# Performance work log

Hardware: AMD Instinct MI355X
Metric: run time of the kernel (lower is better)

## Reference

```python
import jax, jax.numpy as jnp
import numpy as np

B, Ng, A, Eg = 32, 2500, 50, 2000      # graphs, atoms/graph, residues/graph, edges/graph
DIN, EDIM, H1, H2, AF, HG = 64, 16, 64, 64, 95, 128
F1, F2, F3 = 64, 32, 16
K, T = 3, 6                             # ARMA num_stacks, num_layers
N, E = B * Ng, B * Eg


def _glorot(k, shape, fan_in):
    return jax.random.normal(k, shape, jnp.float32) / np.sqrt(fan_in)


def setup_inputs():
    key = jax.random.key(0)
    ks = jax.random.split(key, 24)
    x = jax.random.normal(ks[0], (N, DIN), jnp.float32)
    off = (jnp.arange(B) * Ng)[:, None]
    src = (jax.random.randint(ks[1], (B, Eg), 0, Ng) + off).reshape(-1)
    dst = (jax.random.randint(ks[2], (B, Eg), 0, Ng) + off).reshape(-1)
    edge_index = jnp.stack([src, dst])
    edge_attr = jax.random.normal(ks[3], (E, EDIM), jnp.float32)
    monomer_labels = jnp.tile(jnp.arange(Ng) // (Ng // A), B)  # atom -> residue (0..A-1, per graph)
    aminoacids_features = jax.random.normal(ks[4], (B, A, AF), jnp.float32)
    FIN = H2 + AF  # 159, ARMA input dim
    return {
        'x': x, 'edge_index': edge_index, 'edge_attr': edge_attr,
        'monomer_labels': monomer_labels, 'aminoacids_features': aminoacids_features,
        'w_e1': _glorot(ks[5], (EDIM, DIN * H1), EDIM), 'b_e1': jnp.zeros((DIN * H1,)),
        'root1': _glorot(ks[6], (DIN, H1), DIN), 'bias1': jnp.zeros((H1,)),
        'w_e2': _glorot(ks[7], (EDIM, H1 * H2), EDIM), 'b_e2': jnp.zeros((H1 * H2,)),
        'root2': _glorot(ks[8], (H1, H2), H1), 'bias2': jnp.zeros((H2,)),
        'attn_atom_w': _glorot(ks[9], (H2, 1), H2), 'attn_atom_b': jnp.zeros((1,)),
        'arma_init_w': _glorot(ks[10], (K, FIN, HG), FIN),
        'arma_w': _glorot(ks[11], (T - 1, K, HG, HG), HG),
        'arma_root_w': _glorot(ks[12], (T, K, FIN, HG), FIN),
        'arma_bias': jnp.zeros((T, K, 1, HG)),
        'attn_aa_w': _glorot(ks[13], (HG, 1), HG), 'attn_aa_b': jnp.zeros((1,)),
        'w1': _glorot(ks[14], (HG, F1), HG), 'b1': jnp.zeros((F1,)),
        'w2': _glorot(ks[15], (F1, F2), F1), 'b2': jnp.zeros((F2,)),
        'w3': _glorot(ks[16], (F2, F3), F2), 'b3': jnp.zeros((F3,)),
        'w4': _glorot(ks[17], (F3, 1), F3), 'b4': jnp.zeros((1,)),
    }


def reference(x, edge_index, edge_attr, monomer_labels, aminoacids_features,
              w_e1, b_e1, root1, bias1, w_e2, b_e2, root2, bias2,
              attn_atom_w, attn_atom_b, arma_init_w, arma_w, arma_root_w, arma_bias,
              attn_aa_w, attn_aa_b, w1, b1, w2, b2, w3, b3, w4, b4):
    src, dst = edge_index[0], edge_index[1]

    def nnconv(h, w_e, b_e, root, bias):
        din, dout = root.shape
        W = (edge_attr @ w_e + b_e).reshape(-1, din, dout)      # per-edge weight [E, din, dout]
        msg = jnp.einsum('ei,eio->eo', h[src], W)               # per-edge matvec
        agg = jax.ops.segment_sum(msg, dst, num_segments=N)     # scatter-add at dst
        return agg + h @ root + bias

    h = jax.nn.relu(nnconv(x, w_e1, b_e1, root1, bias1))
    h = jax.nn.relu(nnconv(h, w_e2, b_e2, root2, bias2))

    # AttentionReadoutAtom per graph: softmax over atoms, scatter-sum to residues
    hb = h.reshape(B, Ng, H2)
    attn = jax.nn.softmax(hb @ attn_atom_w + attn_atom_b, axis=1)
    wx = (hb * attn).reshape(-1, H2)
    seg = (monomer_labels.reshape(B, Ng) + jnp.arange(B)[:, None] * A).reshape(-1)
    amino = jax.ops.segment_sum(wx, seg, num_segments=B * A).reshape(B, A, H2)
    xi = jnp.concatenate([amino, aminoacids_features], axis=-1)  # [B, A, H2+95]

    # ARMAConv over directed residue chain i->i+1; gcn_norm w/o self-loops:
    # node 0 has in-degree 0 so edge (0,1) gets norm 0, all others norm 1.
    norm = jnp.concatenate([jnp.zeros(1), jnp.ones(A - 2)])      # [A-1]

    def prop(z):  # z: [B, K, A, F]; out[i+1] = norm_i * z[i]
        shifted = z[..., :-1, :] * norm[:, None]
        return jnp.concatenate([jnp.zeros_like(z[..., :1, :]), shifted], axis=-2)

    out = prop(jnp.einsum('baf,kfg->bkag', xi, arma_init_w))
    out = jax.nn.relu(out + jnp.einsum('baf,kfg->bkag', xi, arma_root_w[0]) + arma_bias[0][None])
    for t in range(1, T):
        out = prop(jnp.einsum('bkaf,kfg->bkag', out, arma_w[t - 1]))
        out = jax.nn.relu(out + jnp.einsum('baf,kfg->bkag', xi, arma_root_w[t]) + arma_bias[t][None])
    g = jax.nn.relu(out.mean(axis=1))  # mean over K stacks -> [B, A, HG]

    # AttentionReadoutAminoAcid: softmax over residues, weighted sum
    a = jax.nn.softmax(g @ attn_aa_w + attn_aa_b, axis=1)
    p = (g * a).sum(axis=1)  # [B, HG]

    # MLP head (dropout is identity in eval mode)
    p = jax.nn.relu(p @ w1 + b1)
    p = jax.nn.relu(p @ w2 + b2)
    p = jax.nn.relu(p @ w3 + b3)
    return (p @ w4 + b4).reshape(-1)
```

## Files before the change

kernel.cpp:

```cpp
#include <hip/hip_runtime.h>

#define N_NODES 80000
#define N_EDGES 64000
#define NB      32
#define NG      2500
#define NA      50
#define EDIM    16
#define FIN     159
#define HG      128
#define RICOLS  2688
#define XSTR    132

typedef __attribute__((ext_vector_type(8))) short bf16x8;
typedef __attribute__((ext_vector_type(4))) float f32x4;

__device__ inline ushort rne_bf16(float f) {
    union { float f; unsigned u; } v; v.f = f;
    const unsigned r = v.u + 0x7fffu + ((v.u >> 16) & 1u);
    return (ushort)(r >> 16);
}
__device__ inline float bf16_to_f32(ushort h) {
    union { unsigned u; float f; } v; v.u = ((unsigned)h) << 16;
    return v.f;
}
__device__ __forceinline__ void gl_lds16(const void* gsrc, void* ldst) {
    __builtin_amdgcn_global_load_lds(
        (const __attribute__((address_space(1))) unsigned int*)gsrc,
        (__attribute__((address_space(3))) unsigned int*)ldst, 16, 0, 0);
}

__global__ __launch_bounds__(256) void prep_w2(const float* __restrict__ we1, const float* __restrict__ be1,
    const float* __restrict__ we2, const float* __restrict__ be2,
    ushort* __restrict__ w1h, ushort* __restrict__ w1l, ushort* __restrict__ w2h, ushort* __restrict__ w2l)
{
    int idx = blockIdx.x * 256 + threadIdx.x;
    const int half = (idx >= 17 * 8 * 64) ? 1 : 0;
    if (half) idx -= 17 * 8 * 64;
    if (idx >= 17 * 8 * 64) return;
    const float* we = half ? we2 : we1;
    const float* be = half ? be2 : be1;
    ushort* Wh = half ? w2h : w1h;
    ushort* Wlo = half ? w2l : w1l;
    const int l = idx & 63;
    const int slot = (idx >> 6) & 7;
    const int j = idx >> 9;
    const int n = slot >> 1, kq = slot & 1;
    const int o = n * 16 + (l & 15);
    const int i0 = kq * 32 + (l >> 4) * 8;
    ushort th[8], tl[8];
#pragma unroll
    for (int t = 0; t < 8; ++t) {
        const int i = i0 + t;
        const float f = (j < 16) ? we[j * 4096 + i * 64 + o] : be[i * 64 + o];
        const ushort hi = rne_bf16(f);
        th[t] = hi;
        tl[t] = rne_bf16(f - bf16_to_f32(hi));
    }
    *(uint4*)(Wh + (size_t)idx * 8) = *(const uint4*)th;
    *(uint4*)(Wlo + (size_t)idx * 8) = *(const uint4*)tl;
}

__global__ __launch_bounds__(256) void prep_arma(const float* __restrict__ armaw,
    ushort* __restrict__ Bh, ushort* __restrict__ Bl)
{
    const int idx = blockIdx.x * 256 + threadIdx.x;
    if (idx >= 15 * 32 * 64) return;
    const int l = idx & 63;
    const int slot = (idx >> 6) & 31;
    const int ws = idx >> 11;
    const int n = slot >> 2, kt = slot & 3;
    const int c = n * 16 + (l & 15);
    const int f0 = kt * 32 + (l >> 4) * 8;
    ushort th[8], tl[8];
#pragma unroll
    for (int t = 0; t < 8; ++t) {
        const float v = armaw[(size_t)ws * 16384 + (size_t)(f0 + t) * 128 + c];
        const ushort hi = rne_bf16(v);
        th[t] = hi;
        tl[t] = rne_bf16(v - bf16_to_f32(hi));
    }
    *(uint4*)(Bh + (size_t)idx * 8) = *(const uint4*)th;
    *(uint4*)(Bl + (size_t)idx * 8) = *(const uint4*)tl;
}

template<int RELU>
__global__ __launch_bounds__(256) void root_gemm(const float* __restrict__ in,
    const float* __restrict__ w, const float* __restrict__ bias, float* __restrict__ out)
{
    __shared__ float At[64 * 65];
    __shared__ float Wl[64 * 64];
    __shared__ float bl[64];
    const int tid = threadIdx.x;
    const int r0 = blockIdx.x * 64;
    for (int s = tid; s < 4096; s += 256) {
        int r = s >> 6, c = s & 63;
        float v = in[(r0 + r) * 64 + c];
        if (RELU) v = fmaxf(v, 0.f);
        At[c * 65 + r] = v;
    }
    for (int s = tid; s < 4096; s += 256) Wl[s] = w[s];
    if (tid < 64) bl[tid] = bias[tid];
    __syncthreads();
    const int tr = tid >> 4, tc = tid & 15;
    float acc[4][4] = {};
#pragma unroll 8
    for (int i = 0; i < 64; ++i) {
        const float4 a4 = *(const float4*)&At[i * 65 + tr * 4];
        const float4 b4 = *(const float4*)&Wl[i * 64 + tc * 4];
        const float av[4] = {a4.x, a4.y, a4.z, a4.w};
        const float bv[4] = {b4.x, b4.y, b4.z, b4.w};
#pragma unroll
        for (int m = 0; m < 4; ++m)
#pragma unroll
            for (int n = 0; n < 4; ++n) acc[m][n] = fmaf(av[m], bv[n], acc[m][n]);
    }
    const float4 bq = *(const float4*)&bl[tc * 4];
#pragma unroll
    for (int m = 0; m < 4; ++m) {
        float4 o4 = {acc[m][0] + bq.x, acc[m][1] + bq.y, acc[m][2] + bq.z, acc[m][3] + bq.w};
        *(float4*)&out[(r0 + tr * 4 + m) * 64 + tc * 4] = o4;
    }
}

#define TE 128
template<int RELU>
__global__ __launch_bounds__(256) void edge_conv_mfma(const float* __restrict__ h,
    const float* __restrict__ ea, const int* __restrict__ src, const int* __restrict__ dst,
    const ushort* __restrict__ Whi, const ushort* __restrict__ Wlo, float* __restrict__ agg)
{
    __shared__ ushort Bst[2][8192];
    __shared__ float  EAt[17 * 132];
    const int tid = threadIdx.x;
    const int e0 = blockIdx.x * TE;
    const int wv = tid >> 6, l = tid & 63;

#pragma unroll
    for (int i = 0; i < 4; ++i) {
        const int c = wv * 4 + i;
        const ushort* gs = (c < 8) ? (Whi + ((size_t)c * 64 + l) * 8)
                                   : (Wlo + ((size_t)(c - 8) * 64 + l) * 8);
        gl_lds16(gs, (char*)(&Bst[0][0]) + c * 1024);
    }
    for (int s = tid; s < TE * 16; s += 256) {
        const int le = s >> 4, j = s & 15;
        EAt[j * 132 + le] = ea[(size_t)(e0 + le) * 16 + j];
    }
    if (tid < TE) EAt[16 * 132 + tid] = 1.0f;

    bf16x8 ah[2][2], al[2][2];
#pragma unroll
    for (int m = 0; m < 2; ++m) {
        const int erow = wv * 32 + m * 16 + (l & 15);
        const int nd = src[e0 + erow];
        const float4* hp = (const float4*)(h + (size_t)nd * 64);
#pragma unroll
        for (int kq = 0; kq < 2; ++kq) {
            const int q0 = kq * 8 + (l >> 4) * 2;
            const float4 v0 = hp[q0], v1 = hp[q0 + 1];
            const float fv[8] = {v0.x, v0.y, v0.z, v0.w, v1.x, v1.y, v1.z, v1.w};
            ushort th[8], tl[8];
#pragma unroll
            for (int t = 0; t < 8; ++t) {
                const float f = RELU ? fmaxf(fv[t], 0.f) : fv[t];
                th[t] = rne_bf16(f);
                tl[t] = rne_bf16(f - bf16_to_f32(th[t]));
            }
            ah[m][kq] = *(const bf16x8*)th;
            al[m][kq] = *(const bf16x8*)tl;
        }
    }
    __syncthreads();

    f32x4 msg[2][4];
#pragma unroll
    for (int m = 0; m < 2; ++m)
#pragma unroll
        for (int n = 0; n < 4; ++n) msg[m][n] = (f32x4)0.f;

#pragma unroll 1
    for (int j = 0; j < 17; ++j) {
        const int cur = j & 1;
        if (j < 16) {
#pragma unroll
            for (int i = 0; i < 4; ++i) {
                const int c = wv * 4 + i;
                const ushort* gs = (c < 8) ? (Whi + ((size_t)((j + 1) * 8 + c) * 64 + l) * 8)
                                           : (Wlo + ((size_t)((j + 1) * 8 + (c - 8)) * 64 + l) * 8);
                gl_lds16(gs, (char*)(&Bst[cur ^ 1][0]) + c * 1024);
            }
        }
        f32x4 eam[2];
        eam[0] = *(const f32x4*)&EAt[j * 132 + wv * 32 + (l >> 4) * 4];
        eam[1] = *(const f32x4*)&EAt[j * 132 + wv * 32 + 16 + (l >> 4) * 4];
#pragma unroll
        for (int n = 0; n < 4; ++n) {
            const char* bb = (const char*)(&Bst[cur][0]);
            const bf16x8 bh0 = *(const bf16x8*)(bb + ((n * 2 + 0) * 64 + l) * 16);
            const bf16x8 bh1 = *(const bf16x8*)(bb + ((n * 2 + 1) * 64 + l) * 16);
            const bf16x8 bl0 = *(const bf16x8*)(bb + 8192 + ((n * 2 + 0) * 64 + l) * 16);
            const bf16x8 bl1 = *(const bf16x8*)(bb + 8192 + ((n * 2 + 1) * 64 + l) * 16);
#pragma unroll
            for (int m = 0; m < 2; ++m) {
                f32x4 t = __builtin_amdgcn_mfma_f32_16x16x32_bf16(ah[m][0], bh0, (f32x4)0.f, 0, 0, 0);
                t = __builtin_amdgcn_mfma_f32_16x16x32_bf16(ah[m][1], bh1, t, 0, 0, 0);
                t = __builtin_amdgcn_mfma_f32_16x16x32_bf16(ah[m][0], bl0, t, 0, 0, 0);
                t = __builtin_amdgcn_mfma_f32_16x16x32_bf16(ah[m][1], bl1, t, 0, 0, 0);
                t = __builtin_amdgcn_mfma_f32_16x16x32_bf16(al[m][0], bh0, t, 0, 0, 0);
                t = __builtin_amdgcn_mfma_f32_16x16x32_bf16(al[m][1], bh1, t, 0, 0, 0);
                msg[m][n] += eam[m] * t;
            }
        }
        __syncthreads();
    }

#pragma unroll
    for (int m = 0; m < 2; ++m)
#pragma unroll
        for (int r = 0; r < 4; ++r) {
            const int erow = wv * 32 + m * 16 + (l >> 4) * 4 + r;
            const size_t d = (size_t)dst[e0 + erow] * 64;
#pragma unroll
            for (int n = 0; n < 4; ++n)
                atomicAdd(&agg[d + n * 16 + (l & 15)], msg[m][n][r]);
        }
}

__global__ __launch_bounds__(256) void scores_k(const float* __restrict__ h2,
    const float* __restrict__ w, const float* __restrict__ b, float* __restrict__ sc)
{
    __shared__ float wl[64];
    if (threadIdx.x < 64) wl[threadIdx.x] = w[threadIdx.x];
    __syncthreads();
    const int n = blockIdx.x * 256 + threadIdx.x;
    if (n < N_NODES) {
        float acc = b[0];
        const float4* hp = (const float4*)(h2 + (long)n * 64);
#pragma unroll
        for (int q = 0; q < 16; ++q) {
            const float4 v = hp[q];
            acc = fmaf(fmaxf(v.x, 0.f), wl[q * 4 + 0], acc); acc = fmaf(fmaxf(v.y, 0.f), wl[q * 4 + 1], acc);
            acc = fmaf(fmaxf(v.z, 0.f), wl[q * 4 + 2], acc); acc = fmaf(fmaxf(v.w, 0.f), wl[q * 4 + 3], acc);
        }
        sc[n] = acc;
    }
}

__global__ __launch_bounds__(256) void softmax_k(const float* __restrict__ sc, float* __restrict__ attn)
{
    __shared__ float red[256];
    const int g = blockIdx.x, tid = threadIdx.x;
    const float* s = sc + (long)g * NG;
    float m = -1e30f;
    for (int a = tid; a < NG; a += 256) m = fmaxf(m, s[a]);
    red[tid] = m; __syncthreads();
    for (int st = 128; st; st >>= 1) { if (tid < st) red[tid] = fmaxf(red[tid], red[tid + st]); __syncthreads(); }
    const float mx = red[0]; __syncthreads();
    float sum = 0.f;
    for (int a = tid; a < NG; a += 256) sum += expf(s[a] - mx);
    red[tid] = sum; __syncthreads();
    for (int st = 128; st; st >>= 1) { if (tid < st) red[tid] += red[tid + st]; __syncthreads(); }
    const float inv = 1.0f / red[0];
    for (int a = tid; a < NG; a += 256) attn[(long)g * NG + a] = expf(s[a] - mx) * inv;
}

__global__ __launch_bounds__(256) void amino_k(const float* __restrict__ h2,
    const float* __restrict__ attn, const float* __restrict__ aa, float* __restrict__ xi)
{
    const int tid = threadIdx.x;
    const int r = blockIdx.x * 4 + (tid >> 6);
    const int o = tid & 63;
    const int g = r / NA, ar = r % NA;
    const long base = (long)g * NG + ar * 50;
    float acc = 0.f;
#pragma unroll 10
    for (int a = 0; a < 50; ++a) acc = fmaf(attn[base + a], fmaxf(h2[(base + a) * 64 + o], 0.f), acc);
    xi[(long)r * FIN + o] = acc;
    for (int s = tid; s < 4 * 95; s += 256) {
        const int lr = s / 95, f = s % 95;
        const int rr = blockIdx.x * 4 + lr;
        xi[(long)rr * FIN + 64 + f] = aa[(long)rr * 95 + f];
    }
}

__global__ __launch_bounds__(256) void ri_gemm(const float* __restrict__ xi,
    const float* __restrict__ rootw, const float* __restrict__ initw,
    const float* __restrict__ abias, float* __restrict__ RI)
{
    __shared__ float At[32 * 65];
    __shared__ float Bl[32 * 64];
    const int tid = threadIdx.x;
    const int r0 = blockIdx.x * 64, c0 = blockIdx.y * 64;
    const int blk = c0 >> 7;
    const int gb = c0 & 127;
    const float* bsrc = (blk < 18) ? (rootw + (long)blk * FIN * 128) : (initw + (long)(blk - 18) * FIN * 128);
    const int tr = tid >> 4, tc = tid & 15;
    float acc[4][4] = {};
    for (int f0 = 0; f0 < FIN; f0 += 32) {
        __syncthreads();
        for (int s = tid; s < 64 * 32; s += 256) {
            const int r = s >> 5, kk = s & 31; const int f = f0 + kk;
            At[kk * 65 + r] = (f < FIN) ? xi[(long)(r0 + r) * FIN + f] : 0.f;
        }
        for (int s = tid; s < 32 * 64; s += 256) {
            const int kk = s >> 6, cc = s & 63; const int f = f0 + kk;
            Bl[s] = (f < FIN) ? bsrc[(long)f * 128 + gb + cc] : 0.f;
        }
        __syncthreads();
#pragma unroll 8
        for (int kk = 0; kk < 32; ++kk) {
            const float4 a4 = *(const float4*)&At[kk * 65 + tr * 4];
            const float4 b4 = *(const float4*)&Bl[kk * 64 + tc * 4];
            const float av[4] = {a4.x, a4.y, a4.z, a4.w};
            const float bv[4] = {b4.x, b4.y, b4.z, b4.w};
#pragma unroll
            for (int m = 0; m < 4; ++m)
#pragma unroll
                for (int n = 0; n < 4; ++n) acc[m][n] = fmaf(av[m], bv[n], acc[m][n]);
        }
    }
    float4 bq = {0.f, 0.f, 0.f, 0.f};
    if (blk < 18) bq = *(const float4*)&abias[c0 + tc * 4];
#pragma unroll
    for (int m = 0; m < 4; ++m) {
        float4 o4 = {acc[m][0] + bq.x, acc[m][1] + bq.y, acc[m][2] + bq.z, acc[m][3] + bq.w};
        *(float4*)&RI[(long)(r0 + tr * 4 + m) * RICOLS + c0 + tc * 4] = o4;
    }
}

__global__ __launch_bounds__(128) void arma_all(const float* __restrict__ RI,
    const ushort* __restrict__ Bh, const ushort* __restrict__ Bl, float* __restrict__ G)
{
    __shared__ float Xl[2][32 * XSTR];
    const int bid = blockIdx.x;
    const int g = bid / 6, k = (bid % 6) >> 1, half = bid & 1;
    const int tid = threadIdx.x;
    const int r0 = half ? 20 : 0;
    const size_t rbase = (size_t)g * NA;

    for (int s = tid; s < 30 * 128; s += 128) {
        const int lr = s >> 7, o = s & 127;
        const int a = r0 + lr;
        float v = RI[(rbase + a) * RICOLS + k * 128 + o];
        if (a >= 2) v += RI[(rbase + a - 1) * RICOLS + (18 + k) * 128 + o];
        Xl[0][lr * XSTR + o] = fmaxf(v, 0.f);
    }
    for (int s = tid; s < 2 * 128; s += 128) {
        const int lr = 30 + (s >> 7), o = s & 127;
        Xl[0][lr * XSTR + o] = 0.f;
        Xl[1][lr * XSTR + o] = 0.f;
    }

    const int wv = tid >> 6, l = tid & 63;
    const int arow = wv * 16 + (l & 15);
    const bool avalid = (arow >= 1) && (r0 + arow >= 2);
    const int asrc = avalid ? (arow - 1) : 0;
    int cur = 0;

    for (int t = 1; t <= 5; ++t) {
        __syncthreads();
        bf16x8 ah[4], al[4];
#pragma unroll
        for (int kt = 0; kt < 4; ++kt) {
            const float* xp = &Xl[cur][asrc * XSTR + kt * 32 + (l >> 4) * 8];
            const float4 v0 = *(const float4*)xp;
            const float4 v1 = *(const float4*)(xp + 4);
            const float fv[8] = {v0.x, v0.y, v0.z, v0.w, v1.x, v1.y, v1.z, v1.w};
            ushort th[8], tl[8];
#pragma unroll
            for (int t8 = 0; t8 < 8; ++t8) {
                const float f = avalid ? fv[t8] : 0.f;
                th[t8] = rne_bf16(f);
                tl[t8] = rne_bf16(f - bf16_to_f32(th[t8]));
            }
            ah[kt] = *(const bf16x8*)th;
            al[kt] = *(const bf16x8*)tl;
        }
        const size_t wsbase = (size_t)(((t - 1) * 3 + k) * 32) * 64 * 8;
#pragma unroll
        for (int n = 0; n < 8; ++n) {
            f32x4 acc = (f32x4)0.f;
#pragma unroll
            for (int kt = 0; kt < 4; ++kt) {
                const size_t fo = wsbase + (size_t)(n * 4 + kt) * 64 * 8 + (size_t)l * 8;
                const bf16x8 bh = *(const bf16x8*)(Bh + fo);
                const bf16x8 bl8 = *(const bf16x8*)(Bl + fo);
                acc = __builtin_amdgcn_mfma_f32_16x16x32_bf16(ah[kt], bh, acc, 0, 0, 0);
                acc = __builtin_amdgcn_mfma_f32_16x16x32_bf16(ah[kt], bl8, acc, 0, 0, 0);
                acc = __builtin_amdgcn_mfma_f32_16x16x32_bf16(al[kt], bh, acc, 0, 0, 0);
            }
            const int cn = n * 16 + (l & 15);
#pragma unroll
            for (int r = 0; r < 4; ++r) {
                const int lr = wv * 16 + (l >> 4) * 4 + r;
                if (lr < 30) {
                    const float rv = RI[(rbase + r0 + lr) * RICOLS + (t * 3 + k) * 128 + cn];
                    Xl[cur ^ 1][lr * XSTR + cn] = fmaxf(acc[r] + rv, 0.f);
                }
            }
        }
        cur ^= 1;
    }
    __syncthreads();
    const int w0 = half ? 25 : 0;
    for (int s = tid; s < 25 * 128; s += 128) {
        const int a = w0 + (s >> 7), o = s & 127;
        G[((size_t)k * 1600 + rbase + a) * 128 + o] = Xl[cur][(a - r0) * XSTR + o];
    }
}

__global__ __launch_bounds__(256) void final_k(const float* __restrict__ G,
    const float* __restrict__ waa, const float* __restrict__ baa,
    const float* __restrict__ w1, const float* __restrict__ b1,
    const float* __restrict__ w2, const float* __restrict__ b2,
    const float* __restrict__ w3, const float* __restrict__ b3,
    const float* __restrict__ w4, const float* __restrict__ b4, float* __restrict__ out)
{
    __shared__ float gl[50 * 129];
    __shared__ float sc[64];
    __shared__ float pl[128];
    __shared__ float h1l[64], h2l[32], h3l[16];
    __shared__ float wl[128];
    const int b = blockIdx.x, tid = threadIdx.x;
    for (int s = tid; s < 50 * 128; s += 256) {
        const int a = s >> 7, o = s & 127;
        const size_t r = ((size_t)b * 50 + a) * 128 + o;
        const float v = (G[r] + G[(size_t)1600 * 128 + r] + G[(size_t)2 * 1600 * 128 + r]) * (1.f / 3.f);
        gl[a * 129 + o] = fmaxf(v, 0.f);
    }
    if (tid < 128) wl[tid] = waa[tid];
    __syncthreads();
    if (tid < 50) {
        float acc = baa[0];
        for (int f = 0; f < 128; ++f) acc = fmaf(gl[tid * 129 + f], wl[f], acc);
        sc[tid] = acc;
    }
    __syncthreads();
    if (tid < 64) {
        const float v = (tid < 50) ? sc[tid] : -1e30f;
        float m = v;
        for (int d = 32; d; d >>= 1) m = fmaxf(m, __shfl_xor(m, d));
        const float e = (tid < 50) ? expf(v - m) : 0.f;
        float ssum = e;
        for (int d = 32; d; d >>= 1) ssum += __shfl_xor(ssum, d);
        if (tid < 50) sc[tid] = e / ssum;
    }
    __syncthreads();
    if (tid < 128) {
        float acc = 0.f;
        for (int a = 0; a < 50; ++a) acc = fmaf(sc[a], gl[a * 129 + tid], acc);
        pl[tid] = acc;
    }
    __syncthreads();
    if (tid < 64) {
        float acc = b1[tid];
        for (int f = 0; f < 128; ++f) acc = fmaf(pl[f], w1[f * 64 + tid], acc);
        h1l[tid] = fmaxf(acc, 0.f);
    }
    __syncthreads();
    if (tid < 32) {
        float acc = b2[tid];
        for (int f = 0; f < 64; ++f) acc = fmaf(h1l[f], w2[f * 32 + tid], acc);
        h2l[tid] = fmaxf(acc, 0.f);
    }
    __syncthreads();
    if (tid < 16) {
        float acc = b3[tid];
        for (int f = 0; f < 32; ++f) acc = fmaf(h2l[f], w3[f * 16 + tid], acc);
        h3l[tid] = fmaxf(acc, 0.f);
    }
    __syncthreads();
    if (tid == 0) {
        float acc = b4[0];
        for (int f = 0; f < 16; ++f) acc = fmaf(h3l[f], w4[f], acc);
        out[b] = acc;
    }
}

extern "C" void kernel_launch(void* const* d_in, const int* in_sizes, int n_in,
                              void* d_out, int out_size, void* d_ws, size_t ws_size,
                              hipStream_t stream) {
    const float* x     = (const float*)d_in[0];
    const int*   eidx  = (const int*)d_in[1];
    const float* ea    = (const float*)d_in[2];
    const float* aaf   = (const float*)d_in[4];
    const float* we1   = (const float*)d_in[5];
    const float* be1   = (const float*)d_in[6];
    const float* root1 = (const float*)d_in[7];
    const float* bias1 = (const float*)d_in[8];
    const float* we2   = (const float*)d_in[9];
    const float* be2   = (const float*)d_in[10];
    const float* root2 = (const float*)d_in[11];
    const float* bias2 = (const float*)d_in[12];
    const float* waw   = (const float*)d_in[13];
    const float* wab   = (const float*)d_in[14];
    const float* initw = (const float*)d_in[15];
    const float* armaw = (const float*)d_in[16];
    const float* rootw = (const float*)d_in[17];
    const float* abias = (const float*)d_in[18];
    const float* waa   = (const float*)d_in[19];
    const float* baa   = (const float*)d_in[20];
    const float* w1    = (const float*)d_in[21];
    const float* b1    = (const float*)d_in[22];
    const float* w2    = (const float*)d_in[23];
    const float* b2    = (const float*)d_in[24];
    const float* w3    = (const float*)d_in[25];
    const float* b3    = (const float*)d_in[26];
    const float* w4    = (const float*)d_in[27];
    const float* b4    = (const float*)d_in[28];
    float* out = (float*)d_out;

    const int* src = eidx;
    const int* dst = eidx + N_EDGES;

    char* ws = (char*)d_ws;
    size_t off = 0;
    float* h1     = (float*)(ws + off); off += (size_t)N_NODES * 64 * 4;
    float* h2     = (float*)(ws + off); off += (size_t)N_NODES * 64 * 4;
    float* scores = (float*)(ws + off); off += (size_t)N_NODES * 4;
    float* attn   = (float*)(ws + off); off += (size_t)N_NODES * 4;
    float* xi     = (float*)(ws + off); off += (size_t)1600 * FIN * 4;
    float* RI     = (float*)(ws + off); off += (size_t)1600 * RICOLS * 4;
    float* G      = (float*)(ws + off); off += (size_t)3 * 1600 * 128 * 4;
    ushort* wt1h  = (ushort*)(ws + off); off += (size_t)17 * 8 * 64 * 8 * 2;
    ushort* wt1l  = (ushort*)(ws + off); off += (size_t)17 * 8 * 64 * 8 * 2;
    ushort* wt2h  = (ushort*)(ws + off); off += (size_t)17 * 8 * 64 * 8 * 2;
    ushort* wt2l  = (ushort*)(ws + off); off += (size_t)17 * 8 * 64 * 8 * 2;
    ushort* abh   = (ushort*)(ws + off); off += (size_t)15 * 32 * 64 * 8 * 2;
    ushort* abl   = (ushort*)(ws + off); off += (size_t)15 * 32 * 64 * 8 * 2;

    prep_w2<<<68, 256, 0, stream>>>(we1, be1, we2, be2, wt1h, wt1l, wt2h, wt2l);
    prep_arma<<<120, 256, 0, stream>>>(armaw, abh, abl);

    root_gemm<0><<<N_NODES / 64, 256, 0, stream>>>(x, root1, bias1, h1);
    edge_conv_mfma<0><<<N_EDGES / TE, 256, 0, stream>>>(x, ea, src, dst, wt1h, wt1l, h1);
    root_gemm<1><<<N_NODES / 64, 256, 0, stream>>>(h1, root2, bias2, h2);
    edge_conv_mfma<1><<<N_EDGES / TE, 256, 0, stream>>>(h1, ea, src, dst, wt2h, wt2l, h2);
    scores_k<<<(N_NODES + 255) / 256, 256, 0, stream>>>(h2, waw, wab, scores);
    softmax_k<<<NB, 256, 0, stream>>>(scores, attn);
    amino_k<<<1600 / 4, 256, 0, stream>>>(h2, attn, aaf, xi);
    ri_gemm<<<dim3(25, 42), 256, 0, stream>>>(xi, rootw, initw, abias, RI);
    arma_all<<<NB * 6, 128, 0, stream>>>(RI, abh, abl, G);
    final_k<<<NB, 256, 0, stream>>>(G, waa, baa, w1, b1, w2, b2, w3, b3, w4, b4, out);
}
```

Baseline: 386.8 us.

## Split ARMA recurrence into single-wave halo chunks and merge weight prep kernels

The ARMA stack kernel is restructured from 192 two-wave blocks with double-buffered LDS and block barriers into 480 single-wave blocks. Each block owns 11 residues plus a 5-row halo, recomputing overlapping rows so that no __syncthreads is needed. The MFMA loop is reordered so that all eight column tiles' B fragments are loaded per k-step and eight independent accumulators are kept, which exposes more instruction-level parallelism at the cost of registers and redundant halo work. The two weight-preparation kernels are also fused into one launch to cut launch overhead.

```diff
diff --git a/kernel.cpp b/kernel.cpp
--- a/kernel.cpp
+++ b/kernel.cpp
@@ -9,7 +9,6 @@
 #define FIN     159
 #define HG      128
 #define RICOLS  2688
-#define XSTR    132
 
 typedef __attribute__((ext_vector_type(8))) short bf16x8;
 typedef __attribute__((ext_vector_type(4))) float f32x4;
@@ -29,58 +28,58 @@
         (__attribute__((address_space(3))) unsigned int*)ldst, 16, 0, 0);
 }
 
-__global__ __launch_bounds__(256) void prep_w2(const float* __restrict__ we1, const float* __restrict__ be1,
-    const float* __restrict__ we2, const float* __restrict__ be2,
-    ushort* __restrict__ w1h, ushort* __restrict__ w1l, ushort* __restrict__ w2h, ushort* __restrict__ w2l)
-{
-    int idx = blockIdx.x * 256 + threadIdx.x;
-    const int half = (idx >= 17 * 8 * 64) ? 1 : 0;
-    if (half) idx -= 17 * 8 * 64;
-    if (idx >= 17 * 8 * 64) return;
-    const float* we = half ? we2 : we1;
-    const float* be = half ? be2 : be1;
-    ushort* Wh = half ? w2h : w1h;
-    ushort* Wlo = half ? w2l : w1l;
-    const int l = idx & 63;
-    const int slot = (idx >> 6) & 7;
-    const int j = idx >> 9;
-    const int n = slot >> 1, kq = slot & 1;
-    const int o = n * 16 + (l & 15);
-    const int i0 = kq * 32 + (l >> 4) * 8;
-    ushort th[8], tl[8];
-#pragma unroll
-    for (int t = 0; t < 8; ++t) {
-        const int i = i0 + t;
-        const float f = (j < 16) ? we[j * 4096 + i * 64 + o] : be[i * 64 + o];
-        const ushort hi = rne_bf16(f);
-        th[t] = hi;
-        tl[t] = rne_bf16(f - bf16_to_f32(hi));
-    }
-    *(uint4*)(Wh + (size_t)idx * 8) = *(const uint4*)th;
-    *(uint4*)(Wlo + (size_t)idx * 8) = *(const uint4*)tl;
-}
-
-__global__ __launch_bounds__(256) void prep_arma(const float* __restrict__ armaw,
-    ushort* __restrict__ Bh, ushort* __restrict__ Bl)
-{
-    const int idx = blockIdx.x * 256 + threadIdx.x;
-    if (idx >= 15 * 32 * 64) return;
-    const int l = idx & 63;
-    const int slot = (idx >> 6) & 31;
-    const int ws = idx >> 11;
-    const int n = slot >> 2, kt = slot & 3;
-    const int c = n * 16 + (l & 15);
-    const int f0 = kt * 32 + (l >> 4) * 8;
-    ushort th[8], tl[8];
-#pragma unroll
-    for (int t = 0; t < 8; ++t) {
-        const float v = armaw[(size_t)ws * 16384 + (size_t)(f0 + t) * 128 + c];
-        const ushort hi = rne_bf16(v);
-        th[t] = hi;
-        tl[t] = rne_bf16(v - bf16_to_f32(hi));
-    }
-    *(uint4*)(Bh + (size_t)idx * 8) = *(const uint4*)th;
-    *(uint4*)(Bl + (size_t)idx * 8) = *(const uint4*)tl;
+__global__ __launch_bounds__(256) void prep_all(const float* __restrict__ we1, const float* __restrict__ be1,
+    const float* __restrict__ we2, const float* __restrict__ be2, const float* __restrict__ armaw,
+    ushort* __restrict__ w1h, ushort* __restrict__ w1l, ushort* __restrict__ w2h, ushort* __restrict__ w2l,
+    ushort* __restrict__ abh, ushort* __restrict__ abl)
+{
+    const int b = blockIdx.x;
+    if (b < 68) {
+        int idx = b * 256 + threadIdx.x;
+        const int half = (idx >= 17 * 8 * 64) ? 1 : 0;
+        if (half) idx -= 17 * 8 * 64;
+        if (idx >= 17 * 8 * 64) return;
+        const float* we = half ? we2 : we1;
+        const float* be = half ? be2 : be1;
+        ushort* Wh = half ? w2h : w1h;
+        ushort* Wlo = half ? w2l : w1l;
+        const int l = idx & 63;
+        const int slot = (idx >> 6) & 7;
+        const int j = idx >> 9;
+        const int n = slot >> 1, kq = slot & 1;
+        const int o = n * 16 + (l & 15);
+        const int i0 = kq * 32 + (l >> 4) * 8;
+        ushort th[8], tl[8];
+#pragma unroll
+        for (int t = 0; t < 8; ++t) {
+            const int i = i0 + t;
+            const float f = (j < 16) ? we[j * 4096 + i * 64 + o] : be[i * 64 + o];
+            const ushort hi = rne_bf16(f);
+            th[t] = hi;
+            tl[t] = rne_bf16(f - bf16_to_f32(hi));
+        }
+        *(uint4*)(Wh + (size_t)idx * 8) = *(const uint4*)th;
+        *(uint4*)(Wlo + (size_t)idx * 8) = *(const uint4*)tl;
+    } else {
+        const int idx = (b - 68) * 256 + threadIdx.x;
+        if (idx >= 15 * 32 * 64) return;
+        const int l = idx & 63;
+        const int slot = (idx >> 6) & 31;
+        const int ws = idx >> 11;
+        const int n = slot >> 2, kt = slot & 3;
+        const int c = n * 16 + (l & 15);
+        const int f0 = kt * 32 + (l >> 4) * 8;
+        ushort th[8], tl[8];
+#pragma unroll
+        for (int t = 0; t < 8; ++t) {
+            const float v = armaw[(size_t)ws * 16384 + (size_t)(f0 + t) * 128 + c];
+            const ushort hi = rne_bf16(v);
+            th[t] = hi;
+            tl[t] = rne_bf16(v - bf16_to_f32(hi));
+        }
+        *(uint4*)(abh + (size_t)idx * 8) = *(const uint4*)th;
+        *(uint4*)(abl + (size_t)idx * 8) = *(const uint4*)tl;
+    }
 }
 
 template<int RELU>
@@ -327,41 +326,41 @@
     }
 }
 
-__global__ __launch_bounds__(128) void arma_all(const float* __restrict__ RI,
+__global__ __launch_bounds__(64) void arma_mfma(const float* __restrict__ RI,
     const ushort* __restrict__ Bh, const ushort* __restrict__ Bl, float* __restrict__ G)
 {
-    __shared__ float Xl[2][32 * XSTR];
+    __shared__ float X[16 * 132];
     const int bid = blockIdx.x;
-    const int g = bid / 6, k = (bid % 6) >> 1, half = bid & 1;
-    const int tid = threadIdx.x;
-    const int r0 = half ? 20 : 0;
+    const int chunk = bid % 5;
+    const int gk = bid / 5;
+    const int k = gk % 3, g = gk / 3;
+    const int s0 = chunk * 11 - 5;
     const size_t rbase = (size_t)g * NA;
-
-    for (int s = tid; s < 30 * 128; s += 128) {
+    const int l = threadIdx.x;
+
+    for (int s = l; s < 16 * 128; s += 64) {
         const int lr = s >> 7, o = s & 127;
-        const int a = r0 + lr;
-        float v = RI[(rbase + a) * RICOLS + k * 128 + o];
-        if (a >= 2) v += RI[(rbase + a - 1) * RICOLS + (18 + k) * 128 + o];
-        Xl[0][lr * XSTR + o] = fmaxf(v, 0.f);
-    }
-    for (int s = tid; s < 2 * 128; s += 128) {
-        const int lr = 30 + (s >> 7), o = s & 127;
-        Xl[0][lr * XSTR + o] = 0.f;
-        Xl[1][lr * XSTR + o] = 0.f;
-    }
-
-    const int wv = tid >> 6, l = tid & 63;
-    const int arow = wv * 16 + (l & 15);
-    const bool avalid = (arow >= 1) && (r0 + arow >= 2);
-    const int asrc = avalid ? (arow - 1) : 0;
-    int cur = 0;
-
+        const int a = s0 + lr;
+        float v = 0.f;
+        if (a >= 0 && a < NA) {
+            v = RI[(rbase + a) * RICOLS + k * 128 + o];
+            if (a >= 2) v += RI[(rbase + a - 1) * RICOLS + (18 + k) * 128 + o];
+            v = fmaxf(v, 0.f);
+        }
+        X[lr * 132 + o] = v;
+    }
+
+    const int arow = l & 15;
+    const int aabs = s0 + arow;
+    const bool avalid = (arow >= 1) && (aabs >= 2) && (aabs < NA);
+    const int srow = avalid ? (arow - 1) : arow;
+
+#pragma unroll 1
     for (int t = 1; t <= 5; ++t) {
-        __syncthreads();
         bf16x8 ah[4], al[4];
 #pragma unroll
         for (int kt = 0; kt < 4; ++kt) {
-            const float* xp = &Xl[cur][asrc * XSTR + kt * 32 + (l >> 4) * 8];
+            const float* xp = &X[srow * 132 + kt * 32 + (l >> 4) * 8];
             const float4 v0 = *(const float4*)xp;
             const float4 v1 = *(const float4*)(xp + 4);
             const float fv[8] = {v0.x, v0.y, v0.z, v0.w, v1.x, v1.y, v1.z, v1.w};
@@ -375,36 +374,47 @@
             ah[kt] = *(const bf16x8*)th;
             al[kt] = *(const bf16x8*)tl;
         }
-        const size_t wsbase = (size_t)(((t - 1) * 3 + k) * 32) * 64 * 8;
+        f32x4 acc[8];
+#pragma unroll
+        for (int n = 0; n < 8; ++n) acc[n] = (f32x4)0.f;
+        const size_t wb = (size_t)(((t - 1) * 3 + k) * 32) * 512;
+#pragma unroll
+        for (int kt = 0; kt < 4; ++kt) {
+            bf16x8 bh8[8], bl8[8];
+#pragma unroll
+            for (int n = 0; n < 8; ++n) {
+                const size_t fo = wb + (size_t)(n * 4 + kt) * 512 + (size_t)l * 8;
+                bh8[n] = *(const bf16x8*)(Bh + fo);
+                bl8[n] = *(const bf16x8*)(Bl + fo);
+            }
+#pragma unroll
+            for (int n = 0; n < 8; ++n) {
+                acc[n] = __builtin_amdgcn_mfma_f32_16x16x32_bf16(ah[kt], bh8[n], acc[n], 0, 0, 0);
+                acc[n] = __builtin_amdgcn_mfma_f32_16x16x32_bf16(ah[kt], bl8[n], acc[n], 0, 0, 0);
+                acc[n] = __builtin_amdgcn_mfma_f32_16x16x32_bf16(al[kt], bh8[n], acc[n], 0, 0, 0);
+            }
+        }
 #pragma unroll
         for (int n = 0; n < 8; ++n) {
-            f32x4 acc = (f32x4)0.f;
-#pragma unroll
-            for (int kt = 0; kt < 4; ++kt) {
-                const size_t fo = wsbase + (size_t)(n * 4 + kt) * 64 * 8 + (size_t)l * 8;
-                const bf16x8 bh = *(const bf16x8*)(Bh + fo);
-                const bf16x8 bl8 = *(const bf16x8*)(Bl + fo);
-                acc = __builtin_amdgcn_mfma_f32_16x16x32_bf16(ah[kt], bh, acc, 0, 0, 0);
-                acc = __builtin_amdgcn_mfma_f32_16x16x32_bf16(ah[kt], bl8, acc, 0, 0, 0);
-                acc = __builtin_amdgcn_mfma_f32_16x16x32_bf16(al[kt], bh, acc, 0, 0, 0);
-            }
-            const int cn = n * 16 + (l & 15);
+            const int col = n * 16 + (l & 15);
 #pragma unroll
             for (int r = 0; r < 4; ++r) {
-                const int lr = wv * 16 + (l >> 4) * 4 + r;
-                if (lr < 30) {
-                    const float rv = RI[(rbase + r0 + lr) * RICOLS + (t * 3 + k) * 128 + cn];
-                    Xl[cur ^ 1][lr * XSTR + cn] = fmaxf(acc[r] + rv, 0.f);
+                const int crow = (l >> 4) * 4 + r;
+                const int ca = s0 + crow;
+                float v = 0.f;
+                if (ca >= 0 && ca < NA) {
+                    const float rv = RI[(rbase + ca) * RICOLS + (t * 3 + k) * 128 + col];
+                    v = fmaxf(acc[n][r] + rv, 0.f);
                 }
-            }
-        }
-        cur ^= 1;
-    }
-    __syncthreads();
-    const int w0 = half ? 25 : 0;
-    for (int s = tid; s < 25 * 128; s += 128) {
-        const int a = w0 + (s >> 7), o = s & 127;
-        G[((size_t)k * 1600 + rbase + a) * 128 + o] = Xl[cur][(a - r0) * XSTR + o];
+                X[crow * 132 + col] = v;
+            }
+        }
+    }
+
+    const int nout = (chunk == 4) ? 6 : 11;
+    for (int s = l; s < nout * 128; s += 64) {
+        const int lr = 5 + (s >> 7), o = s & 127;
+        G[((size_t)k * 1600 + rbase + (size_t)(s0 + lr)) * 128 + o] = X[lr * 132 + o];
     }
 }
 
@@ -528,8 +538,7 @@
     ushort* abh   = (ushort*)(ws + off); off += (size_t)15 * 32 * 64 * 8 * 2;
     ushort* abl   = (ushort*)(ws + off); off += (size_t)15 * 32 * 64 * 8 * 2;
 
-    prep_w2<<<68, 256, 0, stream>>>(we1, be1, we2, be2, wt1h, wt1l, wt2h, wt2l);
-    prep_arma<<<120, 256, 0, stream>>>(armaw, abh, abl);
+    prep_all<<<188, 256, 0, stream>>>(we1, be1, we2, be2, armaw, wt1h, wt1l, wt2h, wt2l, abh, abl);
 
     root_gemm<0><<<N_NODES / 64, 256, 0, stream>>>(x, root1, bias1, h1);
     edge_conv_mfma<0><<<N_EDGES / TE, 256, 0, stream>>>(x, ea, src, dst, wt1h, wt1l, h1);
@@ -539,6 +548,6 @@
     softmax_k<<<NB, 256, 0, stream>>>(scores, attn);
     amino_k<<<1600 / 4, 256, 0, stream>>>(h2, attn, aaf, xi);
     ri_gemm<<<dim3(25, 42), 256, 0, stream>>>(xi, rootw, initw, abias, RI);
-    arma_all<<<NB * 6, 128, 0, stream>>>(RI, abh, abl, G);
+    arma_mfma<<<NB * 3 * 5, 64, 0, stream>>>(RI, abh, abl, G);
     final_k<<<NB, 256, 0, stream>>>(G, waa, baa, w1, b1, w2, b2, w3, b3, w4, b4, out);
 }
```

Measured after the change: 363.1 us. 1.07x faster.
